# Performance work log

Measured on AMD Instinct MI355X. Metric: run time of the kernel, lower is better.

## Reference

```python
import jax, jax.numpy as jnp
import numpy as np

H, C = 8, 16            # heads, per-head channels (at_channels)
HID = H * C             # 128
N_NODES = 50000
N_EDGES = 400000
N_GRAPHS = 500
SPEC = 1000


def setup_inputs() -> dict:
    key = jax.random.key(0)
    ks = jax.random.split(key, 32)
    s = 0.05

    def rn(k, shape):
        return jax.random.normal(k, shape, jnp.float32) * s

    inp = {}
    inp["x"] = jax.random.normal(ks[0], (N_NODES, 16), jnp.float32)
    inp["edge_index"] = jax.random.randint(ks[1], (2, N_EDGES), 0, N_NODES, jnp.int32)
    inp["edge_attr"] = jax.random.normal(ks[2], (N_EDGES, 2), jnp.float32)
    inp["batch"] = jnp.sort(jax.random.randint(ks[3], (N_NODES,), 0, N_GRAPHS, jnp.int32))
    # layer 1 (input dim 16)
    inp["at1_Wl"] = rn(ks[4], (16, HID)); inp["at1_bl"] = rn(ks[5], (HID,))
    inp["at1_Wr"] = rn(ks[6], (16, HID)); inp["at1_br"] = rn(ks[7], (HID,))
    inp["at1_We"] = rn(ks[8], (2, HID))
    inp["at1_att"] = rn(ks[9], (H, C))
    inp["at1_bias"] = rn(ks[10], (HID,))
    inp["l1_W"] = rn(ks[11], (16, HID)); inp["l1_b"] = rn(ks[12], (HID,))
    # layers 2..10 stacked (input dim 128)
    inp["atk_Wl"] = rn(ks[13], (9, HID, HID)); inp["atk_bl"] = rn(ks[14], (9, HID))
    inp["atk_Wr"] = rn(ks[15], (9, HID, HID)); inp["atk_br"] = rn(ks[16], (9, HID))
    inp["atk_We"] = rn(ks[17], (9, 2, HID))
    inp["atk_att"] = rn(ks[18], (9, H, C))
    inp["atk_bias"] = rn(ks[19], (9, HID))
    inp["lk_W"] = rn(ks[20], (9, HID, HID)); inp["lk_b"] = rn(ks[21], (9, HID))
    # readout
    inp["lin_W"] = rn(ks[22], (HID, SPEC)); inp["lin_b"] = rn(ks[23], (SPEC,))
    return inp


def _gatv2(x, src, dst, eattr, Wl, bl, Wr, br, We, att, bias):
    """PyG GATv2Conv forward (concat=True, slope=0.2, self-loops already in src/dst)."""
    N = x.shape[0]
    xl = (x @ Wl + bl).reshape(N, H, C)   # source transform
    xr = (x @ Wr + br).reshape(N, H, C)   # target transform
    ee = (eattr @ We).reshape(-1, H, C)   # edge embedding
    m = xl[src] + xr[dst] + ee            # [E, H, C]
    m = jnp.where(m > 0, m, 0.2 * m)      # leaky_relu
    logits = jnp.einsum('ehc,hc->eh', m, att)
    mx = jax.ops.segment_max(logits, dst, num_segments=N)
    ea = jnp.exp(logits - mx[dst])
    denom = jax.ops.segment_sum(ea, dst, num_segments=N)
    alpha = ea / jnp.maximum(denom[dst], 1e-16)
    out = jax.ops.segment_sum(xl[src] * alpha[:, :, None], dst, num_segments=N)
    return out.reshape(N, HID) + bias


def reference(x, edge_index, edge_attr, batch,
              at1_Wl, at1_bl, at1_Wr, at1_br, at1_We, at1_att, at1_bias, l1_W, l1_b,
              atk_Wl, atk_bl, atk_Wr, atk_br, atk_We, atk_att, atk_bias, lk_W, lk_b,
              lin_W, lin_b):
    N = x.shape[0]
    # add self loops once (edge_attr fill_value='mean', PyG default)
    sl = jnp.arange(N, dtype=edge_index.dtype)
    src = jnp.concatenate([edge_index[0], sl])
    dst = jnp.concatenate([edge_index[1], sl])
    ea = jnp.concatenate([edge_attr, jnp.broadcast_to(edge_attr.mean(0), (N, edge_attr.shape[1]))])

    h = jax.nn.elu(_gatv2(x, src, dst, ea, at1_Wl, at1_bl, at1_Wr, at1_br,
                          at1_We, at1_att, at1_bias) + x @ l1_W + l1_b)
    for i in range(9):  # layers 2..10
        h = jax.nn.elu(_gatv2(h, src, dst, ea, atk_Wl[i], atk_bl[i], atk_Wr[i], atk_br[i],
                              atk_We[i], atk_att[i], atk_bias[i]) + h @ lk_W[i] + lk_b[i])

    # global mean pool over graphs
    sums = jax.ops.segment_sum(h, batch, num_segments=N_GRAPHS)
    cnts = jax.ops.segment_sum(jnp.ones((N, 1), h.dtype), batch, num_segments=N_GRAPHS)
    g = sums / jnp.maximum(cnts, 1.0)
    return g @ lin_W + lin_b
```

## Files before the change

kernel.cpp:

```cpp
#include <hip/hip_runtime.h>
#include <hip/hip_fp16.h>
#include <cstdint>

#define HID 128

typedef __attribute__((ext_vector_type(8))) _Float16 f16x8;
typedef __attribute__((ext_vector_type(2))) _Float16 h2v;
typedef __attribute__((ext_vector_type(4))) float f32x4;

__device__ __forceinline__ unsigned short f2h(float x) {
    return __builtin_bit_cast(unsigned short, (_Float16)x);
}
__device__ __forceinline__ float h2f(unsigned short u) {
    return (float)__builtin_bit_cast(_Float16, u);
}
__device__ __forceinline__ h2v mkh2(unsigned short a, unsigned short b) {
    unsigned v = (unsigned)a | ((unsigned)b << 16);
    return __builtin_bit_cast(h2v, v);
}
__device__ __forceinline__ h2v splath(unsigned short a) {
    _Float16 h = __builtin_bit_cast(_Float16, a);
    h2v r; r[0] = h; r[1] = h;
    return r;
}
__device__ __forceinline__ float fdot2v(h2v a, h2v b, float c) {
    return __builtin_amdgcn_fdot2(a, b, c, false);
}
__device__ __forceinline__ int lower_bound_i(const int* a, int n, int v) {
    int lo = 0, hi = n;
    while (lo < hi) { int m = (lo + hi) >> 1; if (a[m] < v) lo = m + 1; else hi = m; }
    return lo;
}

__global__ __launch_bounds__(256) void mean_kernel(const float* __restrict__ eattr,
                                                   float* __restrict__ meansum, int E) {
    float sx = 0.f, sy = 0.f;
    for (int i = blockIdx.x * 256 + threadIdx.x; i < E; i += gridDim.x * 256) {
        float2 v = *(const float2*)(eattr + 2 * (size_t)i);
        sx += v.x; sy += v.y;
    }
    for (int d = 1; d < 64; d <<= 1) { sx += __shfl_xor(sx, d); sy += __shfl_xor(sy, d); }
    if ((threadIdx.x & 63) == 0) { atomicAdd(&meansum[0], sx); atomicAdd(&meansum[1], sy); }
}

__global__ __launch_bounds__(256) void deg_kernel(const int* __restrict__ ei,
                                                  int* __restrict__ deg, int E, int ET) {
    int e = blockIdx.x * 256 + threadIdx.x;
    if (e >= ET) return;
    int dst = (e < E) ? ei[E + e] : (e - E);
    atomicAdd(&deg[dst], 1);
}

__global__ __launch_bounds__(256) void scanA_kernel(const int* __restrict__ deg,
                                                    int* __restrict__ bsum, int N) {
    __shared__ int ws[4];
    int t = threadIdx.x;
    int base = blockIdx.x * 1024 + t * 4;
    int s = 0;
    #pragma unroll
    for (int j = 0; j < 4; j++) { int idx = base + j; if (idx < N) s += deg[idx]; }
    for (int d = 1; d < 64; d <<= 1) s += __shfl_xor(s, d);
    if ((t & 63) == 0) ws[t >> 6] = s;
    __syncthreads();
    if (t == 0) bsum[blockIdx.x] = ws[0] + ws[1] + ws[2] + ws[3];
}

__global__ __launch_bounds__(64) void scanB_kernel(const int* __restrict__ bsum,
                                                   int* __restrict__ boff,
                                                   int* __restrict__ row_ptr, int NB, int N) {
    int t = threadIdx.x;
    int v = (t < NB) ? bsum[t] : 0;
    int inc = v;
    #pragma unroll
    for (int d = 1; d < 64; d <<= 1) { int u = __shfl_up(inc, d); if (t >= d) inc += u; }
    if (t < NB) boff[t] = inc - v;
    if (t == 63) row_ptr[N] = inc;
}

__global__ __launch_bounds__(256) void scanC_kernel(const int* __restrict__ deg,
                                                    const int* __restrict__ boff,
                                                    int* __restrict__ row_ptr,
                                                    int* __restrict__ cursor, int N) {
    __shared__ int wsum[4];
    int t = threadIdx.x;
    int lane = t & 63, wid = t >> 6;
    int base = blockIdx.x * 1024 + t * 4;
    int v[4]; int s = 0;
    #pragma unroll
    for (int j = 0; j < 4; j++) { int idx = base + j; v[j] = (idx < N) ? deg[idx] : 0; s += v[j]; }
    int inc = s;
    #pragma unroll
    for (int d = 1; d < 64; d <<= 1) { int u = __shfl_up(inc, d); if (lane >= d) inc += u; }
    if (lane == 63) wsum[wid] = inc;
    __syncthreads();
    int woff = 0;
    for (int ww = 0; ww < wid; ww++) woff += wsum[ww];
    int excl = boff[blockIdx.x] + woff + inc - s;
    #pragma unroll
    for (int j = 0; j < 4; j++) {
        int idx = base + j;
        if (idx < N) { row_ptr[idx] = excl; cursor[idx] = excl; }
        excl += v[j];
    }
}

__global__ __launch_bounds__(256) void fill_kernel(const int* __restrict__ ei,
                                                   const float* __restrict__ eattr,
                                                   const float* __restrict__ meansum,
                                                   int* __restrict__ cursor,
                                                   int* __restrict__ csr_src,
                                                   unsigned int* __restrict__ csr_eap,
                                                   int E, int ET) {
    int e = blockIdx.x * 256 + threadIdx.x;
    if (e >= ET) return;
    int src, dst; float2 ea;
    if (e < E) {
        src = ei[e]; dst = ei[E + e];
        ea = *(const float2*)(eattr + 2 * (size_t)e);
    } else {
        src = dst = e - E;
        float inv = 1.0f / (float)E;
        ea.x = meansum[0] * inv; ea.y = meansum[1] * inv;
    }
    unsigned pea = (unsigned)f2h(ea.x) | ((unsigned)f2h(ea.y) << 16);
    int pos = atomicAdd(&cursor[dst], 1);
    csr_src[pos] = src;
    csr_eap[pos] = pea;
}

__global__ __launch_bounds__(256) void wprep_kernel(const float* __restrict__ s0,
                                                    const float* __restrict__ s1,
                                                    const float* __restrict__ s2,
                                                    unsigned short* __restrict__ d0,
                                                    unsigned short* __restrict__ d1,
                                                    unsigned short* __restrict__ d2, int total) {
    int y = blockIdx.y;
    const float* src = (y == 0) ? s0 : (y == 1) ? s1 : s2;
    unsigned short* dst = (y == 0) ? d0 : (y == 1) ? d1 : d2;
    int idx = blockIdx.x * 256 + threadIdx.x;
    if (idx >= total) return;
    int layer = idx >> 14;
    int rem = idx & 16383;
    int n = rem >> 7, k = rem & 127;
    dst[idx] = f2h(src[(layer << 14) | (k << 7) | n]);
}

#define LROW 136
__global__ __launch_bounds__(256) void gemm3_kernel(
    const unsigned short* __restrict__ Hb,
    const unsigned short* __restrict__ W0h, const float* __restrict__ b0, unsigned short* __restrict__ o0,
    const unsigned short* __restrict__ W1h, const float* __restrict__ b1, unsigned short* __restrict__ o1,
    const unsigned short* __restrict__ W2h, const float* __restrict__ b2, unsigned short* __restrict__ o2,
    int N) {
    __shared__ unsigned short lds_h[128 * LROW];
    int tid = threadIdx.x;
    int wid = tid >> 6, lane = tid & 63;
    int row0 = blockIdx.x * 64 + wid * 16;
    int lr = lane & 15;
    int cgrp = lane >> 4;
    int kb = cgrp * 8;
    bool rowsok = (row0 < N);

    f16x8 ha[4];
    {
        int node = row0 + lr;
        int nodec = rowsok ? ((node < N) ? node : (N - 1)) : 0;
        const unsigned short* pa = Hb + (size_t)nodec * HID + kb;
        #pragma unroll
        for (int kf = 0; kf < 4; kf++) ha[kf] = *(const f16x8*)(pa + kf * 32);
    }

    const unsigned short* Whs[3] = {W0h, W1h, W2h};
    const float* Bs[3] = {b0, b1, b2};
    unsigned short* Os[3] = {o0, o1, o2};

    for (int w = 0; w < 3; w++) {
        if (w) __syncthreads();
        const unsigned short* sh = Whs[w];
        #pragma unroll
        for (int j = 0; j < 8; j++) {
            int c = tid + 256 * j;
            int r = c >> 4, col = (c & 15) * 8;
            *(f16x8*)&lds_h[r * LROW + col] = *(const f16x8*)(sh + r * HID + col);
        }
        __syncthreads();
        if (!rowsok) continue;

        const float* bias = Bs[w];
        unsigned short* outp = Os[w];
        #pragma unroll 2
        for (int nf = 0; nf < 8; nf++) {
            int wrow = nf * 16 + lr;
            const unsigned short* ph = &lds_h[wrow * LROW + kb];
            f16x8 wf[4];
            #pragma unroll
            for (int kf = 0; kf < 4; kf++) wf[kf] = *(const f16x8*)(ph + kf * 32);
            f32x4 acc = {0.f, 0.f, 0.f, 0.f};
            #pragma unroll
            for (int kf = 0; kf < 4; kf++)
                acc = __builtin_amdgcn_mfma_f32_16x16x32_f16(wf[kf], ha[kf], acc, 0, 0, 0);
            int chb = nf * 16 + cgrp * 4;
            float4 bias4 = *(const float4*)(bias + chb);
            int node = row0 + lr;
            ushort4 u;
            u.x = f2h(acc[0] + bias4.x); u.y = f2h(acc[1] + bias4.y);
            u.z = f2h(acc[2] + bias4.z); u.w = f2h(acc[3] + bias4.w);
            if (node < N) *(ushort4*)(outp + (size_t)node * HID + chb) = u;
        }
    }
}

__global__ __launch_bounds__(256) void transform16_kernel(
    const float* __restrict__ Hin,
    const float* __restrict__ W0, const float* __restrict__ b0, unsigned short* __restrict__ o0,
    const float* __restrict__ W1, const float* __restrict__ b1, unsigned short* __restrict__ o1,
    int N) {
    constexpr int K = 16;
    __shared__ float Ws[K][HID];
    __shared__ float Hs[32][K + 4];

    const float* W; const float* bias; unsigned short* outp;
    if (blockIdx.z == 0) { W = W0; bias = b0; outp = o0; }
    else                 { W = W1; bias = b1; outp = o1; }

    int row0 = blockIdx.x * 32;
    int tid = threadIdx.x;
    int tx = tid & 15, ty = tid >> 4;

    for (int i = tid; i < 32 * (K / 4); i += 256) {
        int r = i / (K / 4), kq = i % (K / 4);
        int row = row0 + r;
        float4 v = make_float4(0.f, 0.f, 0.f, 0.f);
        if (row < N) v = *(const float4*)(Hin + (size_t)row * K + kq * 4);
        *(float4*)&Hs[r][kq * 4] = v;
    }
    for (int i = tid; i < K * 32; i += 256) {
        int k = i >> 5, cq = i & 31;
        *(float4*)&Ws[k][cq * 4] = *(const float4*)(W + (size_t)k * HID + cq * 4);
    }
    __syncthreads();

    float acc[2][8];
    #pragma unroll
    for (int i = 0; i < 2; i++)
        #pragma unroll
        for (int j = 0; j < 8; j++) acc[i][j] = 0.f;

    int r0 = ty * 2, r1 = ty * 2 + 1;
    #pragma unroll
    for (int k = 0; k < K; k++) {
        float a0 = Hs[r0][k];
        float a1 = Hs[r1][k];
        float4 w0 = *(float4*)&Ws[k][tx * 4];
        float4 w1 = *(float4*)&Ws[k][64 + tx * 4];
        acc[0][0] += a0 * w0.x; acc[0][1] += a0 * w0.y; acc[0][2] += a0 * w0.z; acc[0][3] += a0 * w0.w;
        acc[0][4] += a0 * w1.x; acc[0][5] += a0 * w1.y; acc[0][6] += a0 * w1.z; acc[0][7] += a0 * w1.w;
        acc[1][0] += a1 * w0.x; acc[1][1] += a1 * w0.y; acc[1][2] += a1 * w0.z; acc[1][3] += a1 * w0.w;
        acc[1][4] += a1 * w1.x; acc[1][5] += a1 * w1.y; acc[1][6] += a1 * w1.z; acc[1][7] += a1 * w1.w;
    }

    float4 bb0 = *(const float4*)(bias + tx * 4);
    float4 bb1 = *(const float4*)(bias + 64 + tx * 4);
    #pragma unroll
    for (int i = 0; i < 2; i++) {
        int row = row0 + ty * 2 + i;
        if (row < N) {
            ushort4 h0, h1;
            h0.x = f2h(acc[i][0] + bb0.x); h0.y = f2h(acc[i][1] + bb0.y);
            h0.z = f2h(acc[i][2] + bb0.z); h0.w = f2h(acc[i][3] + bb0.w);
            h1.x = f2h(acc[i][4] + bb1.x); h1.y = f2h(acc[i][5] + bb1.y);
            h1.z = f2h(acc[i][6] + bb1.z); h1.w = f2h(acc[i][7] + bb1.w);
            *(ushort4*)(outp + (size_t)row * HID + tx * 4) = h0;
            *(ushort4*)(outp + (size_t)row * HID + 64 + tx * 4) = h1;
        }
    }
}

__global__ __launch_bounds__(256) void combine16_kernel(
    const float* __restrict__ Hin,
    const float* __restrict__ W, const float* __restrict__ bias,
    const unsigned short* __restrict__ Att, unsigned short* __restrict__ Hb,
    int N) {
    constexpr int K = 16;
    __shared__ float Ws[K][HID];
    __shared__ float Hs[32][K + 4];

    int row0 = blockIdx.x * 32;
    int tid = threadIdx.x;
    int tx = tid & 15, ty = tid >> 4;

    for (int i = tid; i < 32 * (K / 4); i += 256) {
        int r = i / (K / 4), kq = i % (K / 4);
        int row = row0 + r;
        float4 v = make_float4(0.f, 0.f, 0.f, 0.f);
        if (row < N) v = *(const float4*)(Hin + (size_t)row * K + kq * 4);
        *(float4*)&Hs[r][kq * 4] = v;
    }
    for (int i = tid; i < K * 32; i += 256) {
        int k = i >> 5, cq = i & 31;
        *(float4*)&Ws[k][cq * 4] = *(const float4*)(W + (size_t)k * HID + cq * 4);
    }
    __syncthreads();

    float acc[2][8];
    #pragma unroll
    for (int i = 0; i < 2; i++)
        #pragma unroll
        for (int j = 0; j < 8; j++) acc[i][j] = 0.f;

    int r0 = ty * 2, r1 = ty * 2 + 1;
    #pragma unroll
    for (int k = 0; k < K; k++) {
        float a0 = Hs[r0][k];
        float a1 = Hs[r1][k];
        float4 w0 = *(float4*)&Ws[k][tx * 4];
        float4 w1 = *(float4*)&Ws[k][64 + tx * 4];
        acc[0][0] += a0 * w0.x; acc[0][1] += a0 * w0.y; acc[0][2] += a0 * w0.z; acc[0][3] += a0 * w0.w;
        acc[0][4] += a0 * w1.x; acc[0][5] += a0 * w1.y; acc[0][6] += a0 * w1.z; acc[0][7] += a0 * w1.w;
        acc[1][0] += a1 * w0.x; acc[1][1] += a1 * w0.y; acc[1][2] += a1 * w0.z; acc[1][3] += a1 * w0.w;
        acc[1][4] += a1 * w1.x; acc[1][5] += a1 * w1.y; acc[1][6] += a1 * w1.z; acc[1][7] += a1 * w1.w;
    }

    float4 bb0 = *(const float4*)(bias + tx * 4);
    float4 bb1 = *(const float4*)(bias + 64 + tx * 4);
    #pragma unroll
    for (int i = 0; i < 2; i++) {
        int row = row0 + ty * 2 + i;
        if (row < N) {
            const unsigned short* p0 = Att + (size_t)row * HID + tx * 4;
            ushort4 g0 = *(const ushort4*)p0;
            ushort4 g1 = *(const ushort4*)(p0 + 64);
            float v[8];
            v[0] = h2f(g0.x) + acc[i][0] + bb0.x; v[1] = h2f(g0.y) + acc[i][1] + bb0.y;
            v[2] = h2f(g0.z) + acc[i][2] + bb0.z; v[3] = h2f(g0.w) + acc[i][3] + bb0.w;
            v[4] = h2f(g1.x) + acc[i][4] + bb1.x; v[5] = h2f(g1.y) + acc[i][5] + bb1.y;
            v[6] = h2f(g1.z) + acc[i][6] + bb1.z; v[7] = h2f(g1.w) + acc[i][7] + bb1.w;
            #pragma unroll
            for (int j = 0; j < 8; j++) v[j] = (v[j] > 0.f) ? v[j] : (__expf(v[j]) - 1.f);
            ushort4 h0, h1;
            h0.x = f2h(v[0]); h0.y = f2h(v[1]); h0.z = f2h(v[2]); h0.w = f2h(v[3]);
            h1.x = f2h(v[4]); h1.y = f2h(v[5]); h1.z = f2h(v[6]); h1.w = f2h(v[7]);
            *(ushort4*)(Hb + (size_t)row * HID + tx * 4) = h0;
            *(ushort4*)(Hb + (size_t)row * HID + 64 + tx * 4) = h1;
        }
    }
}

template <int FUSE>
__global__ __launch_bounds__(512) void edgeh_kernel(
    const unsigned short* __restrict__ XL, const unsigned short* __restrict__ XR,
    const int* __restrict__ row_ptr, const int* __restrict__ csr_src,
    const unsigned int* __restrict__ csr_eap,
    const float* __restrict__ att,
    const float* __restrict__ We,
    const float* __restrict__ gbias,
    const unsigned short* __restrict__ lin,
    unsigned short* __restrict__ hb,
    int N) {
    int n = (blockIdx.x * 512 + threadIdx.x) >> 6;
    int lane = threadIdx.x & 63;
    int half = lane >> 5;
    int l = lane & 31;
    bool active = (n < N);
    int nn = active ? n : 0;

    int c0 = l * 4;
    float4 avf = *(const float4*)(att + c0);
    float4 w0f = *(const float4*)(We + c0);
    float4 w1f = *(const float4*)(We + HID + c0);
    h2v avA; avA[0] = (_Float16)avf.x; avA[1] = (_Float16)avf.y;
    h2v avB; avB[0] = (_Float16)avf.z; avB[1] = (_Float16)avf.w;
    h2v weA0; weA0[0] = (_Float16)w0f.x; weA0[1] = (_Float16)w0f.y;
    h2v weB0; weB0[0] = (_Float16)w0f.z; weB0[1] = (_Float16)w0f.w;
    h2v weA1; weA1[0] = (_Float16)w1f.x; weA1[1] = (_Float16)w1f.y;
    h2v weB1; weB1[0] = (_Float16)w1f.z; weB1[1] = (_Float16)w1f.w;
    h2v k02; k02[0] = (_Float16)0.2f; k02[1] = (_Float16)0.2f;

    ushort4 xru = *(const ushort4*)(XR + (size_t)nn * HID + c0);
    h2v xrA = mkh2(xru.x, xru.y), xrB = mkh2(xru.z, xru.w);

    int eb = 0, eend = 0;
    if (active) { eb = row_ptr[n]; eend = row_ptr[n + 1]; }
    int mid = (eb + eend + 1) >> 1;
    int sb = half ? mid : eb;
    int se = half ? eend : mid;

    float l_run = 0.f;
    float4 fa = make_float4(0.f, 0.f, 0.f, 0.f);

    for (int base = sb; base < se; base += 32) {
        int cnt = min(32, se - base);
        int myi = base + l;
        int msrc = 0; unsigned mea = 0;
        if (myi < se) { msrc = csr_src[myi]; mea = csr_eap[myi]; }

        int s0 = __shfl(msrc, 0, 32);
        int s1 = __shfl(msrc, 1, 32);
        unsigned e0 = __shfl(mea, 0, 32);
        unsigned e1 = __shfl(mea, 1, 32);
        ushort4 u0 = *(const ushort4*)(XL + (size_t)s0 * HID + c0);
        ushort4 u1 = *(const ushort4*)(XL + (size_t)s1 * HID + c0);

        for (int j = 0; ; j += 2) {
            bool more = (j + 2 < cnt);
            int ns0 = 0, ns1 = 0; unsigned ne0 = 0, ne1 = 0;
            ushort4 nu0, nu1;
            if (more) {
                ns0 = __shfl(msrc, j + 2, 32);
                ns1 = __shfl(msrc, j + 3, 32);
                ne0 = __shfl(mea, j + 2, 32);
                ne1 = __shfl(mea, j + 3, 32);
                nu0 = *(const ushort4*)(XL + (size_t)ns0 * HID + c0);
                nu1 = *(const ushort4*)(XL + (size_t)ns1 * HID + c0);
            }
            h2v ex0 = splath((unsigned short)(e0 & 0xffff));
            h2v ey0 = splath((unsigned short)(e0 >> 16));
            h2v ex1 = splath((unsigned short)(e1 & 0xffff));
            h2v ey1 = splath((unsigned short)(e1 >> 16));
            h2v xl0A = mkh2(u0.x, u0.y), xl0B = mkh2(u0.z, u0.w);
            h2v xl1A = mkh2(u1.x, u1.y), xl1B = mkh2(u1.z, u1.w);

            h2v mA = xl0A + xrA + ex0 * weA0 + ey0 * weA1;
            mA = __builtin_elementwise_max(mA, k02 * mA);
            h2v mB = xl0B + xrB + ex0 * weB0 + ey0 * weB1;
            mB = __builtin_elementwise_max(mB, k02 * mB);
            float part0 = fdot2v(mB, avB, fdot2v(mA, avA, 0.f));

            h2v nA = xl1A + xrA + ex1 * weA0 + ey1 * weA1;
            nA = __builtin_elementwise_max(nA, k02 * nA);
            h2v nB = xl1B + xrB + ex1 * weB0 + ey1 * weB1;
            nB = __builtin_elementwise_max(nB, k02 * nB);
            float part1 = fdot2v(nB, avB, fdot2v(nA, avA, 0.f));

            float t;
            t = __shfl_xor(part0, 1); part0 += t;
            t = __shfl_xor(part0, 2); part0 += t;
            t = __shfl_xor(part1, 1); part1 += t;
            t = __shfl_xor(part1, 2); part1 += t;

            bool two = (j + 1 < cnt);
            float p0 = __expf(fminf(part0, 60.f));
            float p1 = two ? __expf(fminf(part1, 60.f)) : 0.f;
            l_run += p0 + p1;
            fa.x += p0 * h2f(u0.x) + p1 * h2f(u1.x);
            fa.y += p0 * h2f(u0.y) + p1 * h2f(u1.y);
            fa.z += p0 * h2f(u0.z) + p1 * h2f(u1.z);
            fa.w += p0 * h2f(u0.w) + p1 * h2f(u1.w);
            if (!more) break;
            s0 = ns0; s1 = ns1; e0 = ne0; e1 = ne1; u0 = nu0; u1 = nu1;
        }
    }

    l_run += __shfl_xor(l_run, 32);
    fa.x += __shfl_xor(fa.x, 32);
    fa.y += __shfl_xor(fa.y, 32);
    fa.z += __shfl_xor(fa.z, 32);
    fa.w += __shfl_xor(fa.w, 32);

    if (!active || half) return;
    float inv = 1.f / fmaxf(l_run, 1e-16f);
    float4 bias4 = *(const float4*)(gbias + c0);
    float4 v;
    v.x = fa.x * inv + bias4.x;
    v.y = fa.y * inv + bias4.y;
    v.z = fa.z * inv + bias4.z;
    v.w = fa.w * inv + bias4.w;
    if constexpr (FUSE) {
        ushort4 lu = *(const ushort4*)(lin + (size_t)n * HID + c0);
        v.x += h2f(lu.x); v.y += h2f(lu.y); v.z += h2f(lu.z); v.w += h2f(lu.w);
        v.x = (v.x > 0.f) ? v.x : (__expf(v.x) - 1.f);
        v.y = (v.y > 0.f) ? v.y : (__expf(v.y) - 1.f);
        v.z = (v.z > 0.f) ? v.z : (__expf(v.z) - 1.f);
        v.w = (v.w > 0.f) ? v.w : (__expf(v.w) - 1.f);
    }
    ushort4 hh;
    hh.x = f2h(v.x); hh.y = f2h(v.y); hh.z = f2h(v.z); hh.w = f2h(v.w);
    *(ushort4*)(hb + (size_t)n * HID + c0) = hh;
}

__global__ __launch_bounds__(128) void pool_kernel(const unsigned short* __restrict__ h,
                                                   const int* __restrict__ batch,
                                                   float* __restrict__ g, int N) {
    int gid = blockIdx.x;
    int lo = lower_bound_i(batch, N, gid);
    int hi = lower_bound_i(batch, N, gid + 1);
    int c4 = threadIdx.x & 31;
    int sub = threadIdx.x >> 5;
    float4 s = make_float4(0.f, 0.f, 0.f, 0.f);
    for (int i = lo + sub; i < hi; i += 4) {
        ushort4 u = *(const ushort4*)(h + (size_t)i * HID + c4 * 4);
        s.x += h2f(u.x); s.y += h2f(u.y); s.z += h2f(u.z); s.w += h2f(u.w);
    }
    __shared__ float red[4][128];
    *(float4*)&red[sub][c4 * 4] = s;
    __syncthreads();
    if (sub == 0) {
        float4 a = *(float4*)&red[0][c4 * 4];
        float4 b = *(float4*)&red[1][c4 * 4];
        float4 c = *(float4*)&red[2][c4 * 4];
        float4 d = *(float4*)&red[3][c4 * 4];
        float invc = 1.f / fmaxf((float)(hi - lo), 1.0f);
        float4 r;
        r.x = (a.x + b.x + c.x + d.x) * invc;
        r.y = (a.y + b.y + c.y + d.y) * invc;
        r.z = (a.z + b.z + c.z + d.z) * invc;
        r.w = (a.w + b.w + c.w + d.w) * invc;
        *(float4*)(g + (size_t)gid * HID + c4 * 4) = r;
    }
}

__global__ __launch_bounds__(256) void readout_kernel(const float* __restrict__ g,
                                                      const float* __restrict__ W,
                                                      const float* __restrict__ b,
                                                      float* __restrict__ out, int S) {
    __shared__ float gs[HID];
    int gid = blockIdx.y;
    if (threadIdx.x < HID) gs[threadIdx.x] = g[gid * HID + threadIdx.x];
    __syncthreads();
    int c = blockIdx.x * 256 + threadIdx.x;
    if (c < S) {
        float acc = b[c];
        #pragma unroll 8
        for (int k = 0; k < HID; k++) acc += gs[k] * W[(size_t)k * S + c];
        out[(size_t)gid * S + c] = acc;
    }
}

extern "C" void kernel_launch(void* const* d_in, const int* in_sizes, int n_in,
                              void* d_out, int out_size, void* d_ws, size_t ws_size,
                              hipStream_t stream) {
    const float* x      = (const float*)d_in[0];
    const int*   ei     = (const int*)d_in[1];
    const float* eattr  = (const float*)d_in[2];
    const int*   batch  = (const int*)d_in[3];
    const float* at1_Wl = (const float*)d_in[4];
    const float* at1_bl = (const float*)d_in[5];
    const float* at1_Wr = (const float*)d_in[6];
    const float* at1_br = (const float*)d_in[7];
    const float* at1_We = (const float*)d_in[8];
    const float* at1_att= (const float*)d_in[9];
    const float* at1_b  = (const float*)d_in[10];
    const float* l1_W   = (const float*)d_in[11];
    const float* l1_b   = (const float*)d_in[12];
    const float* atk_Wl = (const float*)d_in[13];
    const float* atk_bl = (const float*)d_in[14];
    const float* atk_Wr = (const float*)d_in[15];
    const float* atk_br = (const float*)d_in[16];
    const float* atk_We = (const float*)d_in[17];
    const float* atk_att= (const float*)d_in[18];
    const float* atk_b  = (const float*)d_in[19];
    const float* lk_W   = (const float*)d_in[20];
    const float* lk_b   = (const float*)d_in[21];
    const float* lin_W  = (const float*)d_in[22];
    const float* lin_b  = (const float*)d_in[23];
    float* out = (float*)d_out;

    const int N  = in_sizes[0] / 16;
    const int E  = in_sizes[1] / 2;
    const int ET = E + N;
    const int S  = 1000;
    const int G  = out_size / S;

    char* w = (char*)d_ws;
    auto alloc = [&](size_t bytes) -> char* {
        char* p = w; w += (bytes + 255) & ~(size_t)255; return p;
    };
    unsigned short* XLb = (unsigned short*)alloc((size_t)N * HID * 2);
    unsigned short* XRb = (unsigned short*)alloc((size_t)N * HID * 2);
    unsigned short* Linb = (unsigned short*)alloc((size_t)N * HID * 2);
    unsigned short* Hb = (unsigned short*)alloc((size_t)N * HID * 2);
    int*    deg     = (int*)alloc((size_t)N * 4);
    int*    row_ptr = (int*)alloc((size_t)(N + 1) * 4);
    int*    cursor  = (int*)alloc((size_t)N * 4);
    int*    csr_src = (int*)alloc((size_t)ET * 4);
    unsigned int* csr_eap = (unsigned int*)alloc((size_t)ET * 4);
    float*  meansum = (float*)alloc(8);
    int*    bsum    = (int*)alloc(256);
    int*    boff    = (int*)alloc(256);
    unsigned short* WlTh = (unsigned short*)alloc((size_t)9 * 16384 * 2);
    unsigned short* WrTh = (unsigned short*)alloc((size_t)9 * 16384 * 2);
    unsigned short* WkTh = (unsigned short*)alloc((size_t)9 * 16384 * 2);
    float*  gpool   = (float*)alloc((size_t)G * HID * 4);
    (void)ws_size; (void)n_in;

    hipError_t err;
    err = hipMemsetAsync(deg, 0, (size_t)N * 4, stream); (void)err;
    err = hipMemsetAsync(meansum, 0, 8, stream); (void)err;

    const int wtot = 9 * 16384;
    wprep_kernel<<<dim3((wtot + 255) / 256, 3), 256, 0, stream>>>(atk_Wl, atk_Wr, lk_W,
                                                                  WlTh, WrTh, WkTh, wtot);

    mean_kernel<<<256, 256, 0, stream>>>(eattr, meansum, E);
    deg_kernel<<<(ET + 255) / 256, 256, 0, stream>>>(ei, deg, E, ET);
    const int NB = (N + 1023) / 1024;
    scanA_kernel<<<NB, 256, 0, stream>>>(deg, bsum, N);
    scanB_kernel<<<1, 64, 0, stream>>>(bsum, boff, row_ptr, NB, N);
    scanC_kernel<<<NB, 256, 0, stream>>>(deg, boff, row_ptr, cursor, N);
    fill_kernel<<<(ET + 255) / 256, 256, 0, stream>>>(ei, eattr, meansum, cursor, csr_src, csr_eap, E, ET);

    const int gx16 = (N + 31) / 32;
    const int ge   = (N + 7) / 8;
    const int gx3  = (N + 63) / 64;

    transform16_kernel<<<dim3(gx16, 1, 2), 256, 0, stream>>>(x, at1_Wl, at1_bl, XLb, at1_Wr, at1_br, XRb, N);
    edgeh_kernel<0><<<ge, 512, 0, stream>>>(XLb, XRb, row_ptr, csr_src, csr_eap, at1_att, at1_We, at1_b,
                                            nullptr, Linb, N);
    combine16_kernel<<<gx16, 256, 0, stream>>>(x, l1_W, l1_b, Linb, Hb, N);

    for (int i = 0; i < 9; i++) {
        const unsigned short* wlh = WlTh + (size_t)i * 16384;
        const unsigned short* wrh = WrTh + (size_t)i * 16384;
        const unsigned short* wkh = WkTh + (size_t)i * 16384;
        const float* bl = atk_bl + (size_t)i * HID;
        const float* br = atk_br + (size_t)i * HID;
        const float* bk = lk_b   + (size_t)i * HID;
        const float* Wep = atk_We + (size_t)i * 2 * HID;
        const float* at = atk_att + (size_t)i * HID;
        const float* ab = atk_b  + (size_t)i * HID;

        gemm3_kernel<<<gx3, 256, 0, stream>>>(Hb,
                                              wlh, bl, XLb,
                                              wrh, br, XRb,
                                              wkh, bk, Linb, N);
        edgeh_kernel<1><<<ge, 512, 0, stream>>>(XLb, XRb, row_ptr, csr_src, csr_eap, at, Wep, ab,
                                                Linb, Hb, N);
    }

    pool_kernel<<<G, 128, 0, stream>>>(Hb, batch, gpool, N);
    readout_kernel<<<dim3((S + 255) / 256, G), 256, 0, stream>>>(gpool, lin_W, lin_b, out, S);
}
```

Before: 692.7 us.

## Map one destination node per half-wave in edge kernel; fuse mean and degree kernels

The edge aggregation kernel now assigns each 32-lane half-wave its own destination node instead of splitting one node's edge list across both halves. This halves the grid and drops the cross-half shuffle reduction. The cost is more imbalance, since the two nodes sharing a wave can have different degrees. Separately, the edge-attribute mean and the degree-count kernels are merged into one grid-stride launch, saving a launch at the cost of fewer threads doing the atomics.

```diff
diff --git a/kernel.cpp b/kernel.cpp
--- a/kernel.cpp
+++ b/kernel.cpp
@@ -32,23 +32,22 @@
     return lo;
 }
 
-__global__ __launch_bounds__(256) void mean_kernel(const float* __restrict__ eattr,
-                                                   float* __restrict__ meansum, int E) {
+__global__ __launch_bounds__(256) void meandeg_kernel(const int* __restrict__ ei,
+                                                      const float* __restrict__ eattr,
+                                                      int* __restrict__ deg,
+                                                      float* __restrict__ meansum,
+                                                      int E, int ET) {
     float sx = 0.f, sy = 0.f;
-    for (int i = blockIdx.x * 256 + threadIdx.x; i < E; i += gridDim.x * 256) {
-        float2 v = *(const float2*)(eattr + 2 * (size_t)i);
-        sx += v.x; sy += v.y;
+    for (int i = blockIdx.x * 256 + threadIdx.x; i < ET; i += gridDim.x * 256) {
+        int dst = (i < E) ? ei[E + i] : (i - E);
+        atomicAdd(&deg[dst], 1);
+        if (i < E) {
+            float2 v = *(const float2*)(eattr + 2 * (size_t)i);
+            sx += v.x; sy += v.y;
+        }
     }
     for (int d = 1; d < 64; d <<= 1) { sx += __shfl_xor(sx, d); sy += __shfl_xor(sy, d); }
     if ((threadIdx.x & 63) == 0) { atomicAdd(&meansum[0], sx); atomicAdd(&meansum[1], sy); }
-}
-
-__global__ __launch_bounds__(256) void deg_kernel(const int* __restrict__ ei,
-                                                  int* __restrict__ deg, int E, int ET) {
-    int e = blockIdx.x * 256 + threadIdx.x;
-    if (e >= ET) return;
-    int dst = (e < E) ? ei[E + e] : (e - E);
-    atomicAdd(&deg[dst], 1);
 }
 
 __global__ __launch_bounds__(256) void scanA_kernel(const int* __restrict__ deg,
@@ -357,10 +356,11 @@
     const unsigned short* __restrict__ lin,
     unsigned short* __restrict__ hb,
     int N) {
-    int n = (blockIdx.x * 512 + threadIdx.x) >> 6;
+    int wv = (blockIdx.x * 512 + threadIdx.x) >> 6;
     int lane = threadIdx.x & 63;
     int half = lane >> 5;
     int l = lane & 31;
+    int n = wv * 2 + half;
     bool active = (n < N);
     int nn = active ? n : 0;
 
@@ -379,11 +379,8 @@
     ushort4 xru = *(const ushort4*)(XR + (size_t)nn * HID + c0);
     h2v xrA = mkh2(xru.x, xru.y), xrB = mkh2(xru.z, xru.w);
 
-    int eb = 0, eend = 0;
-    if (active) { eb = row_ptr[n]; eend = row_ptr[n + 1]; }
-    int mid = (eb + eend + 1) >> 1;
-    int sb = half ? mid : eb;
-    int se = half ? eend : mid;
+    int sb = 0, se = 0;
+    if (active) { sb = row_ptr[n]; se = row_ptr[n + 1]; }
 
     float l_run = 0.f;
     float4 fa = make_float4(0.f, 0.f, 0.f, 0.f);
@@ -451,13 +448,7 @@
         }
     }
 
-    l_run += __shfl_xor(l_run, 32);
-    fa.x += __shfl_xor(fa.x, 32);
-    fa.y += __shfl_xor(fa.y, 32);
-    fa.z += __shfl_xor(fa.z, 32);
-    fa.w += __shfl_xor(fa.w, 32);
-
-    if (!active || half) return;
+    if (!active) return;
     float inv = 1.f / fmaxf(l_run, 1e-16f);
     float4 bias4 = *(const float4*)(gbias + c0);
     float4 v;
@@ -591,8 +582,7 @@
     wprep_kernel<<<dim3((wtot + 255) / 256, 3), 256, 0, stream>>>(atk_Wl, atk_Wr, lk_W,
                                                                   WlTh, WrTh, WkTh, wtot);
 
-    mean_kernel<<<256, 256, 0, stream>>>(eattr, meansum, E);
-    deg_kernel<<<(ET + 255) / 256, 256, 0, stream>>>(ei, deg, E, ET);
+    meandeg_kernel<<<256, 256, 0, stream>>>(ei, eattr, deg, meansum, E, ET);
     const int NB = (N + 1023) / 1024;
     scanA_kernel<<<NB, 256, 0, stream>>>(deg, bsum, N);
     scanB_kernel<<<1, 64, 0, stream>>>(bsum, boff, row_ptr, NB, N);
@@ -600,7 +590,7 @@
     fill_kernel<<<(ET + 255) / 256, 256, 0, stream>>>(ei, eattr, meansum, cursor, csr_src, csr_eap, E, ET);
 
     const int gx16 = (N + 31) / 32;
-    const int ge   = (N + 7) / 8;
+    const int ge   = (N + 15) / 16;
     const int gx3  = (N + 63) / 64;
 
     transform16_kernel<<<dim3(gx16, 1, 2), 256, 0, stream>>>(x, at1_Wl, at1_bl, XLb, at1_Wr, at1_br, XRb, N);
```

New measurement: 652.4 us. 5.8% less time.
